# Performance work log

Hardware: AMD Instinct MI355X
Metric: run time of the kernel (lower is better)

Reference implementation:

```python
import jax, jax.numpy as jnp
import numpy as np

EMBED = 1024
HEADS = 16
HEAD_DIM = EMBED // HEADS


def setup_inputs() -> dict:
    key = jax.random.key(0)
    ks = jax.random.split(key, 11)
    B, S, D = 2, 2048, EMBED
    scale = 1.0 / np.sqrt(D)
    inp = {
        "q": jax.random.normal(ks[0], (B, S, D), jnp.float32),
        "k": jax.random.normal(ks[1], (B, S, D), jnp.float32),
        "v": jax.random.normal(ks[2], (B, S, D), jnp.float32),
        "Wq": jax.random.normal(ks[3], (D, D), jnp.float32) * scale,
        "bq": jnp.zeros((D,), jnp.float32),
        "Wk": jax.random.normal(ks[4], (D, D), jnp.float32) * scale,
        "bk": jnp.zeros((D,), jnp.float32),
        "Wv": jax.random.normal(ks[5], (D, D), jnp.float32) * scale,
        "bv": jnp.zeros((D,), jnp.float32),
        "Wo": jax.random.normal(ks[6], (D, D), jnp.float32) * scale,
        "bo": jnp.zeros((D,), jnp.float32),
    }
    return inp


def _split_heads(x):
    b, n, c = x.shape
    return x.reshape(b, n, HEADS, c // HEADS).transpose(0, 2, 1, 3)  # [b,h,n,dh]


def reference(q, k, v, Wq, bq, Wk, bk, Wv, bv, Wo, bo):
    qh = _split_heads(q @ Wq + bq)
    kh = _split_heads(k @ Wk + bk)
    vh = _split_heads(v @ Wv + bv)
    scale = 1.0 / jnp.sqrt(jnp.asarray(HEAD_DIM, qh.dtype))
    att = jnp.einsum("bhqd,bhkd->bhqk", qh, kh) * scale
    att = jax.nn.softmax(att, axis=-1)
    out = jnp.einsum("bhqk,bhkd->bhqd", att, vh)
    b, h, n, dh = out.shape
    out = out.transpose(0, 2, 1, 3).reshape(b, n, h * dh)
    return out @ Wo + bo
```

## Files before the change

### kernel.cpp

```cpp
#include <hip/hip_runtime.h>
#include <hip/hip_bf16.h>
#include <stdint.h>

typedef unsigned short u16;
typedef __bf16 bf16x8 __attribute__((ext_vector_type(8)));
typedef float f32x4 __attribute__((ext_vector_type(4)));
typedef float f32x16 __attribute__((ext_vector_type(16)));
typedef unsigned int u32x4 __attribute__((ext_vector_type(4)));
typedef unsigned int u32x2 __attribute__((ext_vector_type(2)));

#define S_LEN 2048
#define DMODEL 1024
#define NHEAD 16
#define DHEAD 64
#define MROWS 4096
#define EXP2SCALE 0.180336880112f

__device__ __forceinline__ u16 f2b(float f) {
  __hip_bfloat16 h = __float2bfloat16(f);
  union { __hip_bfloat16 h; u16 u; } c;
  c.h = h;
  return c.u;
}
__device__ __forceinline__ unsigned int pk2(float lo, float hi) {
  return (unsigned int)f2b(lo) | ((unsigned int)f2b(hi) << 16);
}
__device__ __forceinline__ unsigned int cvtpk(float a, float b) {
  unsigned int r;
  asm("v_cvt_pk_bf16_f32 %0, %1, %2" : "=v"(r) : "v"(a), "v"(b));
  return r;
}
__device__ __forceinline__ void plswap(unsigned int &a, unsigned int &b) {
  auto r = __builtin_amdgcn_permlane32_swap((int)a, (int)b, false, false);
  a = (unsigned int)r[0];
  b = (unsigned int)r[1];
}

__device__ __forceinline__ void gload16(const void* g, void* l) {
  __builtin_amdgcn_global_load_lds(
      (const __attribute__((address_space(1))) unsigned int*)(uintptr_t)g,
      (__attribute__((address_space(3))) unsigned int*)(uintptr_t)l,
      16, 0, 0);
}

__global__ __launch_bounds__(256) void prep(
    const float* __restrict__ Wq, const float* __restrict__ Wk,
    const float* __restrict__ Wv, const float* __restrict__ Wo,
    u16* __restrict__ Wqt, u16* __restrict__ Wkt,
    u16* __restrict__ Wvt, u16* __restrict__ Wot) {
  __shared__ u16 tile[64][65];
  const int zz = blockIdx.z;
  const int tid = threadIdx.x;
  const float* W = (zz == 0) ? Wq : (zz == 1) ? Wk : (zz == 2) ? Wv : Wo;
  u16* Wt = (zz == 0) ? Wqt : (zz == 1) ? Wkt : (zz == 2) ? Wvt : Wot;
  const int n0 = (blockIdx.x & 15) * 64, k0 = (blockIdx.x >> 4) * 64;
#pragma unroll
  for (int j = 0; j < 16; j++) {
    int idx = j * 256 + tid;
    int r = idx >> 6, c = idx & 63;
    tile[r][c] = f2b(W[(size_t)(k0 + r) * DMODEL + n0 + c]);
  }
  __syncthreads();
#pragma unroll
  for (int j = 0; j < 16; j++) {
    int idx = j * 256 + tid;
    int r = idx >> 6, c = idx & 63;
    Wt[(size_t)(n0 + r) * DMODEL + k0 + c] = tile[c][r];
  }
}

template <int MODE, int AF32>
__device__ __forceinline__ void gemm_body(const void* __restrict__ Av,
                                          const u16* __restrict__ Bt,
                                          const float* __restrict__ bias,
                                          void* __restrict__ Cv,
                                          u16* __restrict__ As,
                                          u16* __restrict__ Bs) {
  constexpr int K = DMODEL;
  const float* Af = (const float*)Av;
  const u16* Ab = (const u16*)Av;
  const int tid = threadIdx.x;
  const int wave = tid >> 6, lane = tid & 63;
  const int quad = lane >> 4, l15 = lane & 15;
  const int wr = wave >> 1, wc = wave & 1;
  const int lid = blockIdx.y * 8 + blockIdx.x;
  const int sw = (lid & 7) * 32 + (lid >> 3);
  const int bcol = sw & 7, brow = sw >> 3;

  f32x4 acc[4][4] = {};
  float4 ar[8];

  if (AF32) {
#pragma unroll
    for (int j = 0; j < 8; j++)
      ar[j] = *(const float4*)(Af +
          (size_t)(brow * 128 + j * 16 + (tid >> 4)) * DMODEL + ((tid & 15) * 4));
  }

  for (int k0 = 0; k0 < K; k0 += 64) {
    __syncthreads();
    if (AF32) {
#pragma unroll
      for (int j = 0; j < 8; j++) {
        const int r = j * 16 + (tid >> 4);
        const int c = (tid & 15) >> 1;
        u32x2 wv;
        wv.x = cvtpk(ar[j].x, ar[j].y);
        wv.y = cvtpk(ar[j].z, ar[j].w);
        *(u32x2*)(As + r * 64 + ((c ^ (r & 7)) << 3) + (tid & 1) * 4) = wv;
      }
#pragma unroll
      for (int t = 0; t < 4; t++) {
        const int slot = t * 256 + wave * 64 + lane;
        const int row = slot >> 3;
        const int cgc = ((slot & 7) ^ (row & 7)) << 3;
        const int ldsb = (t * 256 + wave * 64) * 8;
        gload16(Bt + (size_t)(bcol * 128 + row) * K + k0 + cgc, Bs + ldsb);
      }
    } else {
#pragma unroll
      for (int t = 0; t < 4; t++) {
        const int slot = t * 256 + wave * 64 + lane;
        const int row = slot >> 3;
        const int cgc = ((slot & 7) ^ (row & 7)) << 3;
        const int ldsb = (t * 256 + wave * 64) * 8;
        gload16(Ab + (size_t)(brow * 128 + row) * K + k0 + cgc, As + ldsb);
        gload16(Bt + (size_t)(bcol * 128 + row) * K + k0 + cgc, Bs + ldsb);
      }
    }
    __syncthreads();

    if (AF32 && k0 + 64 < K) {
#pragma unroll
      for (int j = 0; j < 8; j++)
        ar[j] = *(const float4*)(Af +
            (size_t)(brow * 128 + j * 16 + (tid >> 4)) * DMODEL +
            (k0 + 64) + ((tid & 15) * 4));
    }

#pragma unroll
    for (int kk = 0; kk < 2; kk++) {
      bf16x8 af[4], bfm[4];
#pragma unroll
      for (int i = 0; i < 4; i++)
        af[i] = *(const bf16x8*)(As + (wr * 64 + i * 16 + l15) * 64 +
                                 ((((kk << 2) + quad) ^ (l15 & 7)) << 3));
#pragma unroll
      for (int j = 0; j < 4; j++)
        bfm[j] = *(const bf16x8*)(Bs + (wc * 64 + j * 16 + l15) * 64 +
                                  ((((kk << 2) + quad) ^ (l15 & 7)) << 3));
#pragma unroll
      for (int i = 0; i < 4; i++)
#pragma unroll
        for (int j = 0; j < 4; j++)
          acc[i][j] = __builtin_amdgcn_mfma_f32_16x16x32_bf16(af[i], bfm[j], acc[i][j], 0, 0, 0);
    }
  }

#pragma unroll
  for (int i = 0; i < 4; i++)
#pragma unroll
    for (int j = 0; j < 4; j++) {
      const int col = bcol * 128 + wc * 64 + j * 16 + l15;
      const float bv = bias[col];
      if (MODE == 2) {
        const int srow = brow * 128 + wr * 64 + i * 16 + quad * 4;
        const int bb = srow >> 11, s = srow & (S_LEN - 1);
        u32x2 pd;
        pd.x = pk2(acc[i][j][0] + bv, acc[i][j][1] + bv);
        pd.y = pk2(acc[i][j][2] + bv, acc[i][j][3] + bv);
        *(u32x2*)((u16*)Cv + ((size_t)(bb * 1024 + col)) * S_LEN + s) = pd;
      } else {
#pragma unroll
        for (int r = 0; r < 4; r++) {
          const int row = brow * 128 + wr * 64 + i * 16 + quad * 4 + r;
          if (MODE == 1)
            ((float*)Cv)[(size_t)row * DMODEL + col] = acc[i][j][r] + bv;
          else if (MODE == 3)
            ((u16*)Cv)[(size_t)row * DMODEL + col] = f2b((acc[i][j][r] + bv) * EXP2SCALE);
          else
            ((u16*)Cv)[(size_t)row * DMODEL + col] = f2b(acc[i][j][r] + bv);
        }
      }
    }
}

__global__ __launch_bounds__(256, 3) void gemm_qkv(
    const float* __restrict__ q, const float* __restrict__ k, const float* __restrict__ v,
    const u16* __restrict__ Wqt, const u16* __restrict__ Wkt, const u16* __restrict__ Wvt,
    const float* __restrict__ bq, const float* __restrict__ bk, const float* __restrict__ bv,
    u16* __restrict__ Qp, u16* __restrict__ Kp, u16* __restrict__ Vt) {
  __shared__ u16 As[128 * 64];
  __shared__ u16 Bs[128 * 64];
  const int z = blockIdx.z;
  if (z == 2) {
    gemm_body<2, 1>(v, Wvt, bv, Vt, As, Bs);
  } else if (z == 0) {
    gemm_body<3, 1>(q, Wqt, bq, Qp, As, Bs);
  } else {
    gemm_body<0, 1>(k, Wkt, bk, Kp, As, Bs);
  }
}

__global__ __launch_bounds__(256, 4) void gemm_out(
    const u16* __restrict__ A, const u16* __restrict__ Bt,
    const float* __restrict__ bias, float* __restrict__ C) {
  __shared__ u16 As[128 * 64];
  __shared__ u16 Bs[128 * 64];
  gemm_body<1, 0>(A, Bt, bias, C, As, Bs);
}

#define TILE_COMPUTE(ksb, vsb)                                                     \
  do {                                                                             \
    f32x16 sA = {}, sB = {};                                                       \
    __builtin_amdgcn_s_setprio(1);                                                 \
    _Pragma("unroll") for (int c = 0; c < 4; c++) {                                \
      bf16x8 ka0 = *(const bf16x8*)((ksb) + off[c]);                               \
      bf16x8 ka1 = *(const bf16x8*)((ksb) + off[c] + 2048);                        \
      sA = __builtin_amdgcn_mfma_f32_32x32x16_bf16(ka0, qf[c], sA, 0, 0, 0);       \
      sB = __builtin_amdgcn_mfma_f32_32x32x16_bf16(ka1, qf[c], sB, 0, 0, 0);       \
    }                                                                              \
    __builtin_amdgcn_s_setprio(0);                                                 \
    bf16x8 pf[4];                                                                  \
    _Pragma("unroll") for (int kb = 0; kb < 2; kb++) {                             \
      const f32x16 s = kb ? sB : sA;                                               \
      unsigned int cc[8];                                                          \
      _Pragma("unroll") for (int m = 0; m < 8; m++)                                \
        cc[m] = cvtpk(__builtin_amdgcn_exp2f(s[2 * m]),                            \
                      __builtin_amdgcn_exp2f(s[2 * m + 1]));                       \
      plswap(cc[0], cc[2]);                                                        \
      plswap(cc[1], cc[3]);                                                        \
      plswap(cc[4], cc[6]);                                                        \
      plswap(cc[5], cc[7]);                                                        \
      union { unsigned int u[4]; bf16x8 v; } f0, f1;                               \
      f0.u[0] = cc[0]; f0.u[1] = cc[1]; f0.u[2] = cc[2]; f0.u[3] = cc[3];          \
      f1.u[0] = cc[4]; f1.u[1] = cc[5]; f1.u[2] = cc[6]; f1.u[3] = cc[7];          \
      pf[2 * kb] = f0.v; pf[2 * kb + 1] = f1.v;                                    \
    }                                                                              \
    __builtin_amdgcn_s_setprio(1);                                                 \
    _Pragma("unroll") for (int g = 0; g < 4; g++) {                                \
      bf16x8 v0 = *(const bf16x8*)((vsb) + off[g]);                                \
      bf16x8 v1 = *(const bf16x8*)((vsb) + off[g] + 2048);                         \
      lacc  = __builtin_amdgcn_mfma_f32_32x32x16_bf16(pf[g], ones, lacc, 0, 0, 0); \
      oacc0 = __builtin_amdgcn_mfma_f32_32x32x16_bf16(pf[g], v0, oacc0, 0, 0, 0);  \
      oacc1 = __builtin_amdgcn_mfma_f32_32x32x16_bf16(pf[g], v1, oacc1, 0, 0, 0);  \
    }                                                                              \
    __builtin_amdgcn_s_setprio(0);                                                 \
  } while (0)

#define ISSUE(buf, kt)                                                            \
  do {                                                                            \
    if (wave < 4) {                                                               \
      const u16* g = srcK + (size_t)(kt) * 64 * DMODEL;                           \
      _Pragma("unroll") for (int j = 0; j < 4; j++)                               \
        gload16(g + (size_t)j * 8 * DMODEL, dst0 + (buf) * 4096 + j * 512);       \
    } else {                                                                      \
      const u16* g = srcV + (kt) * 64;                                            \
      _Pragma("unroll") for (int j = 0; j < 4; j++)                               \
        gload16(g + (size_t)j * 8 * S_LEN, dst0 + (buf) * 4096 + j * 512);        \
    }                                                                             \
  } while (0)

__global__ __launch_bounds__(512, 4) void attn(const u16* __restrict__ Qp,
                                               const u16* __restrict__ Kp,
                                               const u16* __restrict__ Vt,
                                               u16* __restrict__ Op) {
  __shared__ u16 LB[32768];

  const int tid = threadIdx.x;
  const int wave = tid >> 6, lane = tid & 63;
  const int row31 = lane & 31, hl = lane >> 5;
  const int qg = wave & 3, kh = wave >> 2;

  const int id = blockIdx.x + (blockIdx.y << 4) + (blockIdx.z << 8);
  const int sw = ((id & 7) << 6) + (id >> 3);
  const int qt = sw & 15, h = (sw >> 4) & 15, b = sw >> 8;
  const int s0 = qt * 128;

  const size_t baseK = ((size_t)(b * S_LEN)) * DMODEL + h * DHEAD;
  const size_t baseV = ((size_t)((b * NHEAD + h) * DHEAD)) * S_LEN;

  const int sub = wave & 1, khd = (wave >> 1) & 1;
  const int rl = lane >> 3, cl = lane & 7;
  const int cg8 = (cl ^ rl) << 3;
  const u16* srcK = Kp + baseK + (size_t)(khd * 1024 + sub * 32 + rl) * DMODEL + cg8;
  const u16* srcV = Vt + baseV + (size_t)(sub * 32 + rl) * S_LEN + khd * 1024 + cg8;
  u16* dst0 = LB + (wave >= 4 ? 16384 : 0) + khd * 8192 + (sub * 32) * 64;

  const u16* kcb = LB + kh * 8192;
  const u16* vcb = LB + 16384 + kh * 8192;

  int off[4];
#pragma unroll
  for (int c = 0; c < 4; c++)
    off[c] = row31 * 64 + ((((c << 1) + hl) ^ (row31 & 7)) << 3);

  bf16x8 ones;
  {
    union { u16 a[8]; bf16x8 v; } c;
#pragma unroll
    for (int j = 0; j < 8; j++) c.a[j] = 0x3F80;
    ones = c.v;
  }

  bf16x8 qf[4];
#pragma unroll
  for (int c = 0; c < 4; c++)
    qf[c] = *(const bf16x8*)(Qp +
        ((size_t)(b * S_LEN + s0 + qg * 32 + row31)) * DMODEL +
        h * DHEAD + c * 16 + hl * 8);

  f32x16 oacc0 = {}, oacc1 = {};
  f32x16 lacc = {};

  ISSUE(0, 0);

#pragma unroll 1
  for (int kt = 0; kt < 16; kt += 2) {
    __syncthreads();
    ISSUE(1, kt + 1);
    TILE_COMPUTE(kcb, vcb);
    __syncthreads();
    if (kt + 2 < 16) ISSUE(0, kt + 2);
    TILE_COMPUTE(kcb + 4096, vcb + 4096);
  }

  __syncthreads();
  float* M = ((float*)LB) + qg * 3072;
  if (kh == 1) {
#pragma unroll
    for (int r = 0; r < 16; r++) {
      M[r * 64 + lane]        = oacc0[r];
      M[1024 + r * 64 + lane] = oacc1[r];
      M[2048 + r * 64 + lane] = lacc[r];
    }
  }
  __syncthreads();
  if (kh == 0) {
#pragma unroll
    for (int r = 0; r < 16; r++) {
      const float o0 = oacc0[r] + M[r * 64 + lane];
      const float o1 = oacc1[r] + M[1024 + r * 64 + lane];
      const float ls = lacc[r] + M[2048 + r * 64 + lane];
      const float inv = 1.0f / ls;
      const int qrow = (r & 3) + 8 * (r >> 2) + 4 * hl;
      const size_t rb = ((size_t)(b * S_LEN + s0 + qg * 32 + qrow)) * DMODEL + h * DHEAD;
      Op[rb + row31]      = f2b(o0 * inv);
      Op[rb + 32 + row31] = f2b(o1 * inv);
    }
  }
}

extern "C" void kernel_launch(void* const* d_in, const int* in_sizes, int n_in,
                              void* d_out, int out_size, void* d_ws, size_t ws_size,
                              hipStream_t stream) {
  const float* q  = (const float*)d_in[0];
  const float* k  = (const float*)d_in[1];
  const float* v  = (const float*)d_in[2];
  const float* Wq = (const float*)d_in[3];
  const float* bq = (const float*)d_in[4];
  const float* Wk = (const float*)d_in[5];
  const float* bk = (const float*)d_in[6];
  const float* Wv = (const float*)d_in[7];
  const float* bv = (const float*)d_in[8];
  const float* Wo = (const float*)d_in[9];
  const float* bo = (const float*)d_in[10];

  char* w = (char*)d_ws;
  const size_t WSZ = (size_t)DMODEL * DMODEL * 2;
  const size_t XSZ = (size_t)MROWS * DMODEL * 2;
  u16* Wqt = (u16*)(w);
  u16* Wkt = (u16*)(w + WSZ);
  u16* Wvt = (u16*)(w + 2 * WSZ);
  u16* Wot = (u16*)(w + 3 * WSZ);
  u16* Qp  = (u16*)(w + 4 * WSZ);
  u16* Kp  = (u16*)(w + 4 * WSZ + XSZ);
  u16* Vt  = (u16*)(w + 4 * WSZ + 2 * XSZ);
  u16* Op  = (u16*)(w + 4 * WSZ + 3 * XSZ);

  prep<<<dim3(256, 1, 4), 256, 0, stream>>>(Wq, Wk, Wv, Wo, Wqt, Wkt, Wvt, Wot);
  gemm_qkv<<<dim3(8, 32, 3), 256, 0, stream>>>(q, k, v, Wqt, Wkt, Wvt,
                                               bq, bk, bv, Qp, Kp, Vt);
  attn<<<dim3(16, 16, 2), 512, 0, stream>>>(Qp, Kp, Vt, Op);
  gemm_out<<<dim3(8, 32, 1), 256, 0, stream>>>(Op, Wot, bo, (float*)d_out);
}
```

Baseline: 212.5 us.

## Pre-convert activations to bf16 in prep and shrink output GEMM tile

The prep kernel now also converts the fp32 q/k/v activations to bf16 in a workspace. The QKV GEMM then loads A directly into LDS with async global_load_lds instead of register-staged fp32 loads and in-register conversion, and its occupancy hint rises from 3 to 4. The output projection GEMM uses 64-row M tiles, doubling its grid to 512 blocks for better CU fill. The cost is an extra full write and read of the bf16 activations (about 24MB of traffic) and a larger prep launch.

Measured after the change: 209.5 us. About the same (-1.4%).

```diff
diff --git a/kernel.cpp b/kernel.cpp
--- a/kernel.cpp
+++ b/kernel.cpp
@@ -44,13 +44,29 @@
 }
 
 __global__ __launch_bounds__(256) void prep(
+    const float* __restrict__ q, const float* __restrict__ k, const float* __restrict__ v,
     const float* __restrict__ Wq, const float* __restrict__ Wk,
     const float* __restrict__ Wv, const float* __restrict__ Wo,
+    u16* __restrict__ Qx, u16* __restrict__ Kx, u16* __restrict__ Vx,
     u16* __restrict__ Wqt, u16* __restrict__ Wkt,
     u16* __restrict__ Wvt, u16* __restrict__ Wot) {
   __shared__ u16 tile[64][65];
-  const int zz = blockIdx.z;
+  const int z = blockIdx.z;
   const int tid = threadIdx.x;
+  if (z < 3) {
+    const float* src = (z == 0) ? q : (z == 1) ? k : v;
+    u16* dst = (z == 0) ? Qx : (z == 1) ? Kx : Vx;
+    const size_t i8 = ((size_t)blockIdx.x * 256 + tid) * 8;
+    float4 a = *(const float4*)(src + i8);
+    float4 b = *(const float4*)(src + i8 + 4);
+    u16 o[8];
+    o[0] = f2b(a.x); o[1] = f2b(a.y); o[2] = f2b(a.z); o[3] = f2b(a.w);
+    o[4] = f2b(b.x); o[5] = f2b(b.y); o[6] = f2b(b.z); o[7] = f2b(b.w);
+    *(u32x4*)(dst + i8) = *(const u32x4*)o;
+    return;
+  }
+  if (blockIdx.x >= 256) return;
+  const int zz = z - 3;
   const float* W = (zz == 0) ? Wq : (zz == 1) ? Wk : (zz == 2) ? Wv : Wo;
   u16* Wt = (zz == 0) ? Wqt : (zz == 1) ? Wkt : (zz == 2) ? Wvt : Wot;
   const int n0 = (blockIdx.x & 15) * 64, k0 = (blockIdx.x >> 4) * 64;
@@ -69,88 +85,60 @@
   }
 }
 
-template <int MODE, int AF32>
-__device__ __forceinline__ void gemm_body(const void* __restrict__ Av,
+template <int MODE, int BM>
+__device__ __forceinline__ void gemm_body(const u16* __restrict__ A,
                                           const u16* __restrict__ Bt,
                                           const float* __restrict__ bias,
                                           void* __restrict__ Cv,
                                           u16* __restrict__ As,
                                           u16* __restrict__ Bs) {
   constexpr int K = DMODEL;
-  const float* Af = (const float*)Av;
-  const u16* Ab = (const u16*)Av;
+  constexpr int MB = MROWS / BM;
+  constexpr int TA = BM / 32;
+  constexpr int NI = BM / 32;
   const int tid = threadIdx.x;
   const int wave = tid >> 6, lane = tid & 63;
   const int quad = lane >> 4, l15 = lane & 15;
   const int wr = wave >> 1, wc = wave & 1;
   const int lid = blockIdx.y * 8 + blockIdx.x;
-  const int sw = (lid & 7) * 32 + (lid >> 3);
+  const int sw = (lid & 7) * MB + (lid >> 3);
   const int bcol = sw & 7, brow = sw >> 3;
 
-  f32x4 acc[4][4] = {};
-  float4 ar[8];
-
-  if (AF32) {
-#pragma unroll
-    for (int j = 0; j < 8; j++)
-      ar[j] = *(const float4*)(Af +
-          (size_t)(brow * 128 + j * 16 + (tid >> 4)) * DMODEL + ((tid & 15) * 4));
-  }
+  f32x4 acc[NI][4] = {};
 
   for (int k0 = 0; k0 < K; k0 += 64) {
     __syncthreads();
-    if (AF32) {
-#pragma unroll
-      for (int j = 0; j < 8; j++) {
-        const int r = j * 16 + (tid >> 4);
-        const int c = (tid & 15) >> 1;
-        u32x2 wv;
-        wv.x = cvtpk(ar[j].x, ar[j].y);
-        wv.y = cvtpk(ar[j].z, ar[j].w);
-        *(u32x2*)(As + r * 64 + ((c ^ (r & 7)) << 3) + (tid & 1) * 4) = wv;
-      }
-#pragma unroll
-      for (int t = 0; t < 4; t++) {
-        const int slot = t * 256 + wave * 64 + lane;
-        const int row = slot >> 3;
-        const int cgc = ((slot & 7) ^ (row & 7)) << 3;
-        const int ldsb = (t * 256 + wave * 64) * 8;
-        gload16(Bt + (size_t)(bcol * 128 + row) * K + k0 + cgc, Bs + ldsb);
-      }
-    } else {
-#pragma unroll
-      for (int t = 0; t < 4; t++) {
-        const int slot = t * 256 + wave * 64 + lane;
-        const int row = slot >> 3;
-        const int cgc = ((slot & 7) ^ (row & 7)) << 3;
-        const int ldsb = (t * 256 + wave * 64) * 8;
-        gload16(Ab + (size_t)(brow * 128 + row) * K + k0 + cgc, As + ldsb);
-        gload16(Bt + (size_t)(bcol * 128 + row) * K + k0 + cgc, Bs + ldsb);
-      }
+#pragma unroll
+    for (int t = 0; t < TA; t++) {
+      const int slot = t * 256 + wave * 64 + lane;
+      const int row = slot >> 3;
+      const int cgc = ((slot & 7) ^ (row & 7)) << 3;
+      const int ldsb = (t * 256 + wave * 64) * 8;
+      gload16(A + (size_t)(brow * BM + row) * K + k0 + cgc, As + ldsb);
+    }
+#pragma unroll
+    for (int t = 0; t < 4; t++) {
+      const int slot = t * 256 + wave * 64 + lane;
+      const int row = slot >> 3;
+      const int cgc = ((slot & 7) ^ (row & 7)) << 3;
+      const int ldsb = (t * 256 + wave * 64) * 8;
+      gload16(Bt + (size_t)(bcol * 128 + row) * K + k0 + cgc, Bs + ldsb);
     }
     __syncthreads();
 
-    if (AF32 && k0 + 64 < K) {
-#pragma unroll
-      for (int j = 0; j < 8; j++)
-        ar[j] = *(const float4*)(Af +
-            (size_t)(brow * 128 + j * 16 + (tid >> 4)) * DMODEL +
-            (k0 + 64) + ((tid & 15) * 4));
-    }
-
 #pragma unroll
     for (int kk = 0; kk < 2; kk++) {
-      bf16x8 af[4], bfm[4];
-#pragma unroll
-      for (int i = 0; i < 4; i++)
-        af[i] = *(const bf16x8*)(As + (wr * 64 + i * 16 + l15) * 64 +
+      bf16x8 af[NI], bfm[4];
+#pragma unroll
+      for (int i = 0; i < NI; i++)
+        af[i] = *(const bf16x8*)(As + (wr * (BM / 2) + i * 16 + l15) * 64 +
                                  ((((kk << 2) + quad) ^ (l15 & 7)) << 3));
 #pragma unroll
       for (int j = 0; j < 4; j++)
         bfm[j] = *(const bf16x8*)(Bs + (wc * 64 + j * 16 + l15) * 64 +
                                   ((((kk << 2) + quad) ^ (l15 & 7)) << 3));
 #pragma unroll
-      for (int i = 0; i < 4; i++)
+      for (int i = 0; i < NI; i++)
 #pragma unroll
         for (int j = 0; j < 4; j++)
           acc[i][j] = __builtin_amdgcn_mfma_f32_16x16x32_bf16(af[i], bfm[j], acc[i][j], 0, 0, 0);
@@ -158,13 +146,13 @@
   }
 
 #pragma unroll
-  for (int i = 0; i < 4; i++)
+  for (int i = 0; i < NI; i++)
 #pragma unroll
     for (int j = 0; j < 4; j++) {
       const int col = bcol * 128 + wc * 64 + j * 16 + l15;
       const float bv = bias[col];
       if (MODE == 2) {
-        const int srow = brow * 128 + wr * 64 + i * 16 + quad * 4;
+        const int srow = brow * BM + wr * (BM / 2) + i * 16 + quad * 4;
         const int bb = srow >> 11, s = srow & (S_LEN - 1);
         u32x2 pd;
         pd.x = pk2(acc[i][j][0] + bv, acc[i][j][1] + bv);
@@ -173,7 +161,7 @@
       } else {
 #pragma unroll
         for (int r = 0; r < 4; r++) {
-          const int row = brow * 128 + wr * 64 + i * 16 + quad * 4 + r;
+          const int row = brow * BM + wr * (BM / 2) + i * 16 + quad * 4 + r;
           if (MODE == 1)
             ((float*)Cv)[(size_t)row * DMODEL + col] = acc[i][j][r] + bv;
           else if (MODE == 3)
@@ -185,8 +173,8 @@
     }
 }
 
-__global__ __launch_bounds__(256, 3) void gemm_qkv(
-    const float* __restrict__ q, const float* __restrict__ k, const float* __restrict__ v,
+__global__ __launch_bounds__(256, 4) void gemm_qkv(
+    const u16* __restrict__ Qx, const u16* __restrict__ Kx, const u16* __restrict__ Vx,
     const u16* __restrict__ Wqt, const u16* __restrict__ Wkt, const u16* __restrict__ Wvt,
     const float* __restrict__ bq, const float* __restrict__ bk, const float* __restrict__ bv,
     u16* __restrict__ Qp, u16* __restrict__ Kp, u16* __restrict__ Vt) {
@@ -194,20 +182,20 @@
   __shared__ u16 Bs[128 * 64];
   const int z = blockIdx.z;
   if (z == 2) {
-    gemm_body<2, 1>(v, Wvt, bv, Vt, As, Bs);
+    gemm_body<2, 128>(Vx, Wvt, bv, Vt, As, Bs);
   } else if (z == 0) {
-    gemm_body<3, 1>(q, Wqt, bq, Qp, As, Bs);
+    gemm_body<3, 128>(Qx, Wqt, bq, Qp, As, Bs);
   } else {
-    gemm_body<0, 1>(k, Wkt, bk, Kp, As, Bs);
+    gemm_body<0, 128>(Kx, Wkt, bk, Kp, As, Bs);
   }
 }
 
 __global__ __launch_bounds__(256, 4) void gemm_out(
     const u16* __restrict__ A, const u16* __restrict__ Bt,
     const float* __restrict__ bias, float* __restrict__ C) {
-  __shared__ u16 As[128 * 64];
+  __shared__ u16 As[64 * 64];
   __shared__ u16 Bs[128 * 64];
-  gemm_body<1, 0>(A, Bt, bias, C, As, Bs);
+  gemm_body<1, 64>(A, Bt, bias, C, As, Bs);
 }
 
 #define TILE_COMPUTE(ksb, vsb)                                                     \
@@ -373,14 +361,18 @@
   u16* Wkt = (u16*)(w + WSZ);
   u16* Wvt = (u16*)(w + 2 * WSZ);
   u16* Wot = (u16*)(w + 3 * WSZ);
-  u16* Qp  = (u16*)(w + 4 * WSZ);
-  u16* Kp  = (u16*)(w + 4 * WSZ + XSZ);
-  u16* Vt  = (u16*)(w + 4 * WSZ + 2 * XSZ);
-  u16* Op  = (u16*)(w + 4 * WSZ + 3 * XSZ);
-
-  prep<<<dim3(256, 1, 4), 256, 0, stream>>>(Wq, Wk, Wv, Wo, Wqt, Wkt, Wvt, Wot);
-  gemm_qkv<<<dim3(8, 32, 3), 256, 0, stream>>>(q, k, v, Wqt, Wkt, Wvt,
+  u16* Qx  = (u16*)(w + 4 * WSZ);
+  u16* Kx  = (u16*)(w + 4 * WSZ + XSZ);
+  u16* Vx  = (u16*)(w + 4 * WSZ + 2 * XSZ);
+  u16* Qp  = (u16*)(w + 4 * WSZ + 3 * XSZ);
+  u16* Kp  = (u16*)(w + 4 * WSZ + 4 * XSZ);
+  u16* Vt  = (u16*)(w + 4 * WSZ + 5 * XSZ);
+  u16* Op  = (u16*)(w + 4 * WSZ + 6 * XSZ);
+
+  prep<<<dim3(2048, 1, 7), 256, 0, stream>>>(q, k, v, Wq, Wk, Wv, Wo,
+                                             Qx, Kx, Vx, Wqt, Wkt, Wvt, Wot);
+  gemm_qkv<<<dim3(8, 32, 3), 256, 0, stream>>>(Qx, Kx, Vx, Wqt, Wkt, Wvt,
                                                bq, bk, bv, Qp, Kp, Vt);
   attn<<<dim3(16, 16, 2), 512, 0, stream>>>(Qp, Kp, Vt, Op);
-  gemm_out<<<dim3(8, 32, 1), 256, 0, stream>>>(Op, Wot, bo, (float*)d_out);
-}
+  gemm_out<<<dim3(8, 64, 1), 256, 0, stream>>>(Op, Wot, bo, (float*)d_out);
+}
```
